# Performance work log

Hardware: AMD Instinct MI355X
Metric: run time of the kernel (lower is better)

The kernel has to match this reference:

```python
import jax, jax.numpy as jnp
import numpy as np

LEAK = 0.1   # LeakyReLU negative slope used by Conv2dBatchLeaky
EPS = 1e-5   # BatchNorm eps (torch default)


def conv_bn_leaky(x, w, gamma, beta, mean, var, stride, pad):
    # Conv2d(bias=False) -> BatchNorm (inference) -> LeakyReLU(0.1)
    y = jax.lax.conv_general_dilated(
        x, w, (stride, stride), [(pad, pad), (pad, pad)],
        dimension_numbers=("NCHW", "OIHW", "NCHW"))
    scale = gamma / jnp.sqrt(var + EPS)
    shift = beta - mean * scale
    y = y * scale[None, :, None, None] + shift[None, :, None, None]
    return jnp.where(y > 0, y, LEAK * y)


def reorg(x, s):
    # lightnet Reorg: exact permutation of the darknet reorg layer
    B, C, H, W = x.shape
    x = x.reshape(B, C, H // s, s, W // s, s)
    x = x.transpose(0, 3, 5, 1, 2, 4)           # (B, s, s, C, H/s, W/s)
    return x.reshape(B, s * s * C, H // s, W // s)


def setup_inputs() -> dict:
    key = jax.random.key(0)
    ks = jax.random.split(key, 13)
    B = 64
    inp = {
        "feat0": jax.random.normal(ks[0], (B, 1024, 19, 19), jnp.float32),
        "feat1": jax.random.normal(ks[1], (B, 512, 38, 38), jnp.float32),
        "w1": jax.random.normal(ks[2], (64, 512, 1, 1), jnp.float32) * 0.05,
        "g1": jax.random.uniform(ks[3], (64,), jnp.float32, 0.5, 1.5),
        "b1": jax.random.normal(ks[4], (64,), jnp.float32) * 0.1,
        "m1": jax.random.normal(ks[5], (64,), jnp.float32) * 0.1,
        "v1": jax.random.uniform(ks[6], (64,), jnp.float32, 0.5, 1.5),
        "w2": jax.random.normal(ks[7], (1024, 1280, 3, 3), jnp.float32) * 0.02,
        "g2": jax.random.uniform(ks[8], (1024,), jnp.float32, 0.5, 1.5),
        "b2": jax.random.normal(ks[9], (1024,), jnp.float32) * 0.1,
        "m2": jax.random.normal(ks[10], (1024,), jnp.float32) * 0.1,
        "v2": jax.random.uniform(ks[11], (1024,), jnp.float32, 0.5, 1.5),
        # meta_state: (num_classes=20, num_anchors*6=30, 1024+1)
        "reweight": jax.random.normal(ks[12], (20, 30, 1025), jnp.float32) * 0.05,
    }
    return inp


def reference(feat0, feat1, w1, g1, b1, m1, v1, w2, g2, b2, m2, v2, reweight):
    # layers[0]: 1x1 ConvBatchLeaky(512->64) + Reorg(2)
    x = conv_bn_leaky(feat1, w1, g1, b1, m1, v1, stride=1, pad=0)
    x = reorg(x, 2)                                  # (B, 256, 19, 19)
    # layers[1]: 3x3 ConvBatchLeaky(1280->1024), pad=1
    cat = jnp.concatenate([x, feat0], axis=1)        # (B, 1280, 19, 19)
    pre = conv_bn_leaky(cat, w2, g2, b2, m2, v2, stride=1, pad=1)  # (B,1024,19,19)
    # get_reweighted_output: per-class dynamic 1x1 conv, batched as one einsum
    cw = reweight[:, :, :-1]                         # (K=20, O=30, 1024)
    cb = reweight[:, :, -1]                          # (K, O)
    det = jnp.einsum("bchw,koc->bkohw", pre, cw) + cb[None, :, :, None, None]
    B, _, _, H, W = det.shape
    return det.reshape(B * 20, 30, H, W)
```

## Files before the change

### kernel.cpp

```cpp
#include <hip/hip_runtime.h>

typedef unsigned short u16;
typedef __attribute__((ext_vector_type(8))) __bf16 bf16x8;
typedef __attribute__((ext_vector_type(4))) float f32x4;

__device__ __forceinline__ u16 f2bf(float f) {
  union { float f; unsigned u; } v; v.f = f;
  unsigned r = v.u + 0x7fffu + ((v.u >> 16) & 1u);
  return (u16)(r >> 16);
}

__device__ __forceinline__ void gld16(const void* g, const void* l) {
  __builtin_amdgcn_global_load_lds((const __attribute__((address_space(1))) void*)g,
                                   (__attribute__((address_space(3))) void*)l, 16, 0, 0);
}


__global__ __launch_bounds__(256) void k_prep_params(
    const float* g1, const float* b1, const float* m1, const float* v1,
    const float* g2, const float* b2, const float* m2, const float* v2,
    const float* rw, float* scale1, float* shift1, float* scale2, float* shift2,
    float* cbf)
{
  int i = blockIdx.x * 256 + threadIdx.x;
  if (i < 64) {
    float s = g1[i] * rsqrtf(v1[i] + 1e-5f);
    scale1[i] = s; shift1[i] = b1[i] - m1[i] * s;
  } else if (i < 1088) {
    int c = i - 64;
    float s = g2[c] * rsqrtf(v2[c] + 1e-5f);
    scale2[c] = s; shift2[c] = b2[c] - m2[c] * s;
  } else if (i < 1728) {
    int n = i - 1088;
    cbf[n] = (n < 600) ? rw[n * 1025 + 1024] : 0.f;
  }
}

__global__ __launch_bounds__(256) void k_cast_w1(const float* w1, u16* w1b) {
  int i = blockIdx.x * 256 + threadIdx.x;
  w1b[i] = f2bf(w1[i]);
}

__global__ __launch_bounds__(256) void k_cast_cwt(const float* rw, u16* cwt) {
  int i = blockIdx.x * 256 + threadIdx.x;
  int n = i >> 10, c = i & 1023;
  cwt[i] = (n < 600) ? f2bf(rw[n * 1025 + c]) : (u16)0;
}

__global__ __launch_bounds__(256) void k_prep_w2(const float* w2, u16* w2t) {
  __shared__ float buf[11520];
  int o = blockIdx.x;
  const float* src = w2 + (size_t)o * 11520;
  for (int i = threadIdx.x; i < 11520; i += 256) buf[i] = src[i];
  __syncthreads();
  for (int t = 0; t < 9; ++t) {
    u16* dst = w2t + ((size_t)t * 1024 + o) * 1280;
    for (int ci = threadIdx.x; ci < 1280; ci += 256) dst[ci] = f2bf(buf[ci * 9 + t]);
  }
}

__global__ __launch_bounds__(256) void k_feat0(const float* feat0, u16* cat) {
  __shared__ float tile[32][33];
  int b = blockIdx.z, c0 = blockIdx.y * 32, p0 = blockIdx.x * 32;
  int tid = threadIdx.x;
  int lo = tid & 31, hi = tid >> 5;
#pragma unroll
  for (int pass = 0; pass < 4; ++pass) {
    int cl = pass * 8 + hi;
    int p = p0 + lo;
    tile[cl][lo] = (p < 361) ? feat0[((size_t)(b * 1024 + c0 + cl)) * 361 + p] : 0.f;
  }
  __syncthreads();
#pragma unroll
  for (int pass = 0; pass < 4; ++pass) {
    int pl = pass * 8 + hi;
    int p = p0 + pl;
    if (p < 361) {
      int h = p / 19, w = p - h * 19;
      cat[(((size_t)b * 21 + 1 + h) * 21 + 1 + w) * 1280 + 256 + c0 + lo] = f2bf(tile[lo][pl]);
    }
  }
}

__global__ __launch_bounds__(256) void k_conv1(const float* feat1, const u16* w1b,
    const float* scale1, const float* shift1, u16* cat)
{
  __shared__ u16 As[128 * 40];
  __shared__ u16 Bs[64 * 32];
  int tid = threadIdx.x;
  int wave = tid >> 6, lane = tid & 63;
  int wr = wave >> 1, wc = wave & 1;
  int lm = lane & 15, lq = lane >> 4;
  int m0 = blockIdx.x * 128;

  int mLoc = tid & 127, cHalf = tid >> 7;
  int mA = m0 + mLoc;
  int bA = mA / 1444, qA = mA - bA * 1444;
  const float* aG = feat1 + ((size_t)bA * 512) * 1444 + qA;

  const u16* bG = w1b + (tid >> 2) * 512 + (tid & 3) * 8;
  char* BsW = (char*)Bs + wave * 1024;

  f32x4 acc[4][2];
#pragma unroll
  for (int i = 0; i < 4; ++i)
#pragma unroll
    for (int j = 0; j < 2; ++j)
#pragma unroll
      for (int r = 0; r < 4; ++r) acc[i][j][r] = 0.f;

  for (int k0 = 0; k0 < 512; k0 += 32) {
    gld16(bG + k0, BsW);
#pragma unroll
    for (int pass = 0; pass < 16; ++pass) {
      int c = pass * 2 + cHalf;
      As[mLoc * 40 + c] = f2bf(aG[(size_t)(k0 + c) * 1444]);
    }
    __syncthreads();
    bf16x8 aF[4], bF[2];
#pragma unroll
    for (int i = 0; i < 4; ++i)
      aF[i] = *(const bf16x8*)(As + (wr * 64 + i * 16 + lm) * 40 + lq * 8);
#pragma unroll
    for (int j = 0; j < 2; ++j)
      bF[j] = *(const bf16x8*)(Bs + (wc * 32 + j * 16 + lm) * 32 + lq * 8);
#pragma unroll
    for (int i = 0; i < 4; ++i)
#pragma unroll
      for (int j = 0; j < 2; ++j)
        acc[i][j] = __builtin_amdgcn_mfma_f32_16x16x32_bf16(aF[i], bF[j], acc[i][j], 0, 0, 0);
    __syncthreads();
  }

  int o0 = wc * 32;
  float sc[2], sh[2];
#pragma unroll
  for (int j = 0; j < 2; ++j) {
    int o = o0 + j * 16 + lm;
    sc[j] = scale1[o]; sh[j] = shift1[o];
  }
#pragma unroll
  for (int i = 0; i < 4; ++i) {
#pragma unroll
    for (int r = 0; r < 4; ++r) {
      int m = m0 + wr * 64 + i * 16 + lq * 4 + r;
      int b = m / 1444, q = m - b * 1444;
      int yy = q / 38, xx = q - yy * 38;
      size_t base = (((size_t)b * 21 + 1 + (yy >> 1)) * 21 + 1 + (xx >> 1)) * 1280
                  + ((yy & 1) * 2 + (xx & 1)) * 64;
#pragma unroll
      for (int j = 0; j < 2; ++j) {
        float v = acc[i][j][r] * sc[j] + sh[j];
        v = v > 0.f ? v : 0.1f * v;
        cat[base + o0 + j * 16 + lm] = f2bf(v);
      }
    }
  }
}

__global__ __launch_bounds__(256) void k_conv2(const u16* cat, const u16* w2t,
    const float* scale2, const float* shift2, u16* pre)
{
  __shared__ u16 As[4096];
  __shared__ u16 Bs[4096];
  int tid = threadIdx.x;
  int wave = tid >> 6, lane = tid & 63;
  int wr = wave >> 1, wc = wave & 1;
  int lm = lane & 15, lq = lane >> 4;
  int n0 = blockIdx.x * 128, m0 = blockIdx.y * 128;

  int r0 = tid >> 2, seg = tid & 3;
  int mA0 = m0 + r0;       if (mA0 > 23103) mA0 = 23103;
  int mA1 = m0 + r0 + 64;  if (mA1 > 23103) mA1 = 23103;
  int b0 = mA0 / 361, p0 = mA0 - b0 * 361, y0 = p0 / 19, x0 = p0 - y0 * 19;
  int b1 = mA1 / 361, p1 = mA1 - b1 * 361, y1 = p1 / 19, x1 = p1 - y1 * 19;
  const u16* aP0 = cat + ((size_t)(b0 * 21 + y0) * 21 + x0) * 1280 + seg * 8;
  const u16* aP1 = cat + ((size_t)(b1 * 21 + y1) * 21 + x1) * 1280 + seg * 8;
  const u16* bP0 = w2t + (size_t)(n0 + r0) * 1280 + seg * 8;
  const u16* bP1 = bP0 + (size_t)64 * 1280;

  char* AsW0 = (char*)As + wave * 1024; char* AsW1 = AsW0 + 4096;
  char* BsW0 = (char*)Bs + wave * 1024; char* BsW1 = BsW0 + 4096;

  f32x4 acc[4][4];
#pragma unroll
  for (int i = 0; i < 4; ++i)
#pragma unroll
    for (int j = 0; j < 4; ++j)
#pragma unroll
      for (int r = 0; r < 4; ++r) acc[i][j][r] = 0.f;

#pragma unroll
  for (int t = 0; t < 9; ++t) {
    const int tapOff = ((t / 3) * 21 + (t % 3)) * 1280;
    const u16* a0 = aP0 + tapOff;
    const u16* a1 = aP1 + tapOff;
    const u16* bb0 = bP0 + (size_t)t * 1310720;
    const u16* bb1 = bP1 + (size_t)t * 1310720;
    for (int k = 0; k < 40; ++k) {
      int co = k * 32;
      gld16(a0 + co, AsW0);
      gld16(a1 + co, AsW1);
      gld16(bb0 + co, BsW0);
      gld16(bb1 + co, BsW1);
      __syncthreads();
      bf16x8 aF[4], bF[4];
#pragma unroll
      for (int i = 0; i < 4; ++i)
        aF[i] = *(const bf16x8*)(As + (wr * 64 + i * 16 + lm) * 32 + lq * 8);
#pragma unroll
      for (int j = 0; j < 4; ++j)
        bF[j] = *(const bf16x8*)(Bs + (wc * 64 + j * 16 + lm) * 32 + lq * 8);
#pragma unroll
      for (int i = 0; i < 4; ++i)
#pragma unroll
        for (int j = 0; j < 4; ++j)
          acc[i][j] = __builtin_amdgcn_mfma_f32_16x16x32_bf16(aF[i], bF[j], acc[i][j], 0, 0, 0);
      __syncthreads();
    }
  }

  int nn[4]; float sc[4], sh[4];
#pragma unroll
  for (int j = 0; j < 4; ++j) {
    nn[j] = n0 + wc * 64 + j * 16 + lm;
    sc[j] = scale2[nn[j]]; sh[j] = shift2[nn[j]];
  }
#pragma unroll
  for (int i = 0; i < 4; ++i) {
#pragma unroll
    for (int r = 0; r < 4; ++r) {
      int m = m0 + wr * 64 + i * 16 + lq * 4 + r;
      if (m < 23104) {
        u16* row = pre + (size_t)m * 1024;
#pragma unroll
        for (int j = 0; j < 4; ++j) {
          float v = acc[i][j][r] * sc[j] + sh[j];
          v = v > 0.f ? v : 0.1f * v;
          row[nn[j]] = f2bf(v);
        }
      }
    }
  }
}

__global__ __launch_bounds__(256) void k_einsum(const u16* pre, const u16* cwt,
    const float* cbf, float* out)
{
  __shared__ u16 As[4096];
  __shared__ u16 Bs[4096];
  int tid = threadIdx.x;
  int wave = tid >> 6, lane = tid & 63;
  int wr = wave >> 1, wc = wave & 1;
  int lm = lane & 15, lq = lane >> 4;
  int n0 = blockIdx.x * 128, m0 = blockIdx.y * 128;

  int r0 = tid >> 2, seg = tid & 3;
  int mA0 = m0 + r0;       if (mA0 > 23103) mA0 = 23103;
  int mA1 = m0 + r0 + 64;  if (mA1 > 23103) mA1 = 23103;
  const u16* aP0 = pre + (size_t)mA0 * 1024 + seg * 8;
  const u16* aP1 = pre + (size_t)mA1 * 1024 + seg * 8;
  const u16* bP0 = cwt + (size_t)(n0 + r0) * 1024 + seg * 8;
  const u16* bP1 = bP0 + (size_t)64 * 1024;

  char* AsW0 = (char*)As + wave * 1024; char* AsW1 = AsW0 + 4096;
  char* BsW0 = (char*)Bs + wave * 1024; char* BsW1 = BsW0 + 4096;

  f32x4 acc[4][4];
#pragma unroll
  for (int i = 0; i < 4; ++i)
#pragma unroll
    for (int j = 0; j < 4; ++j)
#pragma unroll
      for (int r = 0; r < 4; ++r) acc[i][j][r] = 0.f;

  for (int k0 = 0; k0 < 1024; k0 += 32) {
    gld16(aP0 + k0, AsW0);
    gld16(aP1 + k0, AsW1);
    gld16(bP0 + k0, BsW0);
    gld16(bP1 + k0, BsW1);
    __syncthreads();
    bf16x8 aF[4], bF[4];
#pragma unroll
    for (int i = 0; i < 4; ++i)
      aF[i] = *(const bf16x8*)(As + (wr * 64 + i * 16 + lm) * 32 + lq * 8);
#pragma unroll
    for (int j = 0; j < 4; ++j)
      bF[j] = *(const bf16x8*)(Bs + (wc * 64 + j * 16 + lm) * 32 + lq * 8);
#pragma unroll
    for (int i = 0; i < 4; ++i)
#pragma unroll
      for (int j = 0; j < 4; ++j)
        acc[i][j] = __builtin_amdgcn_mfma_f32_16x16x32_bf16(aF[i], bF[j], acc[i][j], 0, 0, 0);
    __syncthreads();
  }

  int nn[4]; float bias[4];
#pragma unroll
  for (int j = 0; j < 4; ++j) {
    nn[j] = n0 + wc * 64 + j * 16 + lm;
    bias[j] = cbf[nn[j]];
  }
#pragma unroll
  for (int i = 0; i < 4; ++i) {
#pragma unroll
    for (int r = 0; r < 4; ++r) {
      int m = m0 + wr * 64 + i * 16 + lq * 4 + r;
      if (m < 23104) {
        int b = m / 361, p = m - b * 361;
        float* orow = out + (size_t)b * 600 * 361 + p;
#pragma unroll
        for (int j = 0; j < 4; ++j) {
          if (nn[j] < 600) orow[(size_t)nn[j] * 361] = acc[i][j][r] + bias[j];
        }
      }
    }
  }
}


extern "C" void kernel_launch(void* const* d_in, const int* in_sizes, int n_in,
                              void* d_out, int out_size, void* d_ws, size_t ws_size,
                              hipStream_t stream) {
  const float* feat0 = (const float*)d_in[0];
  const float* feat1 = (const float*)d_in[1];
  const float* w1 = (const float*)d_in[2];
  const float* g1 = (const float*)d_in[3];
  const float* b1 = (const float*)d_in[4];
  const float* m1 = (const float*)d_in[5];
  const float* v1 = (const float*)d_in[6];
  const float* w2 = (const float*)d_in[7];
  const float* g2 = (const float*)d_in[8];
  const float* b2 = (const float*)d_in[9];
  const float* m2 = (const float*)d_in[10];
  const float* v2 = (const float*)d_in[11];
  const float* rw = (const float*)d_in[12];
  float* out = (float*)d_out;

  char* ws = (char*)d_ws;
  u16* cat    = (u16*)(ws);
  u16* w2t    = (u16*)(ws + 72253440);
  u16* pre    = (u16*)(ws + 95846400);
  u16* w1b    = (u16*)(ws + 143163392);
  u16* cwt    = (u16*)(ws + 143228928);
  float* scale1 = (float*)(ws + 144539648);
  float* shift1 = (float*)(ws + 144539904);
  float* scale2 = (float*)(ws + 144540160);
  float* shift2 = (float*)(ws + 144544256);
  float* cbf    = (float*)(ws + 144548352);

  hipMemsetAsync(cat, 0, 72253440, stream);

  k_prep_params<<<7, 256, 0, stream>>>(g1, b1, m1, v1, g2, b2, m2, v2, rw,
                                       scale1, shift1, scale2, shift2, cbf);
  k_cast_w1<<<128, 256, 0, stream>>>(w1, w1b);
  k_cast_cwt<<<2560, 256, 0, stream>>>(rw, cwt);
  k_prep_w2<<<1024, 256, 0, stream>>>(w2, w2t);
  k_feat0<<<dim3(12, 32, 64), 256, 0, stream>>>(feat0, cat);
  k_conv1<<<722, 256, 0, stream>>>(feat1, w1b, scale1, shift1, cat);
  k_conv2<<<dim3(8, 181), 256, 0, stream>>>(cat, w2t, scale2, shift2, pre);
  k_einsum<<<dim3(5, 181), 256, 0, stream>>>(pre, cwt, cbf, out);
}
```

Measured before the change: 1.348 ms.

## Merge dx taps into contiguous K, double K-step in conv2, transpose einsum operands

The conv2 weights are reordered so the three dx taps of each kernel row sit next to each other (K=3840 per dy). This works because neighbouring x pixels in the padded NHWC cat buffer are contiguous, so each dy becomes a single long GEMM K loop. The conv2 main loop now loads 64 K-elements per barrier pair instead of 32, which halves the synchronisation count and doubles LDS usage. The einsum swaps operands so class weights are the M dimension and pixels the N dimension. Output writes then become coalesced along pixels instead of strided by 361, and the grid changes to match.

Measured after the change: 1.219 ms. -9.6%, faster.

```diff
diff --git a/kernel.cpp b/kernel.cpp
--- a/kernel.cpp
+++ b/kernel.cpp
@@ -54,7 +54,8 @@
   for (int i = threadIdx.x; i < 11520; i += 256) buf[i] = src[i];
   __syncthreads();
   for (int t = 0; t < 9; ++t) {
-    u16* dst = w2t + ((size_t)t * 1024 + o) * 1280;
+    int dy = t / 3, dx = t - dy * 3;
+    u16* dst = w2t + ((size_t)dy * 1024 + o) * 3840 + dx * 1280;
     for (int ci = threadIdx.x; ci < 1280; ci += 256) dst[ci] = f2bf(buf[ci * 9 + t]);
   }
 }
@@ -161,26 +162,31 @@
 __global__ __launch_bounds__(256) void k_conv2(const u16* cat, const u16* w2t,
     const float* scale2, const float* shift2, u16* pre)
 {
-  __shared__ u16 As[4096];
-  __shared__ u16 Bs[4096];
+  __shared__ u16 As[8192];
+  __shared__ u16 Bs[8192];
   int tid = threadIdx.x;
   int wave = tid >> 6, lane = tid & 63;
   int wr = wave >> 1, wc = wave & 1;
   int lm = lane & 15, lq = lane >> 4;
   int n0 = blockIdx.x * 128, m0 = blockIdx.y * 128;
 
-  int r0 = tid >> 2, seg = tid & 3;
-  int mA0 = m0 + r0;       if (mA0 > 23103) mA0 = 23103;
-  int mA1 = m0 + r0 + 64;  if (mA1 > 23103) mA1 = 23103;
-  int b0 = mA0 / 361, p0 = mA0 - b0 * 361, y0 = p0 / 19, x0 = p0 - y0 * 19;
-  int b1 = mA1 / 361, p1 = mA1 - b1 * 361, y1 = p1 / 19, x1 = p1 - y1 * 19;
-  const u16* aP0 = cat + ((size_t)(b0 * 21 + y0) * 21 + x0) * 1280 + seg * 8;
-  const u16* aP1 = cat + ((size_t)(b1 * 21 + y1) * 21 + x1) * 1280 + seg * 8;
-  const u16* bP0 = w2t + (size_t)(n0 + r0) * 1280 + seg * 8;
-  const u16* bP1 = bP0 + (size_t)64 * 1280;
-
-  char* AsW0 = (char*)As + wave * 1024; char* AsW1 = AsW0 + 4096;
-  char* BsW0 = (char*)Bs + wave * 1024; char* BsW1 = BsW0 + 4096;
+  int rIn = lane >> 2;
+  int kseg = (lane & 3) * 8;
+  int rowLo = wave * 16 + rIn;
+
+  int mLo = m0 + rowLo;       if (mLo > 23103) mLo = 23103;
+  int mHi = m0 + rowLo + 64;  if (mHi > 23103) mHi = 23103;
+  int bL = mLo / 361, pL = mLo - bL * 361, yL = pL / 19, xL = pL - yL * 19;
+  int bH = mHi / 361, pH = mHi - bH * 361, yH = pH / 19, xH = pH - yH * 19;
+  const u16* aLo = cat + ((size_t)(bL * 21 + yL) * 21 + xL) * 1280 + kseg;
+  const u16* aHi = cat + ((size_t)(bH * 21 + yH) * 21 + xH) * 1280 + kseg;
+  const u16* bLo = w2t + (size_t)(n0 + rowLo) * 3840 + kseg;
+  const u16* bHi = bLo + (size_t)64 * 3840;
+
+  u16* asJ0 = As + wave * 512;          u16* asJ1 = As + (4 + wave) * 512;
+  u16* asJ2 = As + 4096 + wave * 512;   u16* asJ3 = As + 4096 + (4 + wave) * 512;
+  u16* bsJ0 = Bs + wave * 512;          u16* bsJ1 = Bs + (4 + wave) * 512;
+  u16* bsJ2 = Bs + 4096 + wave * 512;   u16* bsJ3 = Bs + 4096 + (4 + wave) * 512;
 
   f32x4 acc[4][4];
 #pragma unroll
@@ -190,32 +196,36 @@
 #pragma unroll
       for (int r = 0; r < 4; ++r) acc[i][j][r] = 0.f;
 
-#pragma unroll
-  for (int t = 0; t < 9; ++t) {
-    const int tapOff = ((t / 3) * 21 + (t % 3)) * 1280;
-    const u16* a0 = aP0 + tapOff;
-    const u16* a1 = aP1 + tapOff;
-    const u16* bb0 = bP0 + (size_t)t * 1310720;
-    const u16* bb1 = bP1 + (size_t)t * 1310720;
-    for (int k = 0; k < 40; ++k) {
-      int co = k * 32;
-      gld16(a0 + co, AsW0);
-      gld16(a1 + co, AsW1);
-      gld16(bb0 + co, BsW0);
-      gld16(bb1 + co, BsW1);
+  for (int dy = 0; dy < 3; ++dy) {
+    const u16* a0 = aLo + dy * 26880;
+    const u16* a1 = aHi + dy * 26880;
+    const u16* b0 = bLo + (size_t)dy * 3932160;
+    const u16* b1 = bHi + (size_t)dy * 3932160;
+    for (int k0 = 0; k0 < 3840; k0 += 64) {
+      gld16(a0 + k0,      asJ0);
+      gld16(a1 + k0,      asJ1);
+      gld16(a0 + k0 + 32, asJ2);
+      gld16(a1 + k0 + 32, asJ3);
+      gld16(b0 + k0,      bsJ0);
+      gld16(b1 + k0,      bsJ1);
+      gld16(b0 + k0 + 32, bsJ2);
+      gld16(b1 + k0 + 32, bsJ3);
       __syncthreads();
-      bf16x8 aF[4], bF[4];
-#pragma unroll
-      for (int i = 0; i < 4; ++i)
-        aF[i] = *(const bf16x8*)(As + (wr * 64 + i * 16 + lm) * 32 + lq * 8);
-#pragma unroll
-      for (int j = 0; j < 4; ++j)
-        bF[j] = *(const bf16x8*)(Bs + (wc * 64 + j * 16 + lm) * 32 + lq * 8);
-#pragma unroll
-      for (int i = 0; i < 4; ++i)
+#pragma unroll
+      for (int kk = 0; kk < 2; ++kk) {
+        bf16x8 aF[4], bF[4];
+#pragma unroll
+        for (int i = 0; i < 4; ++i)
+          aF[i] = *(const bf16x8*)(As + kk * 4096 + (wr * 64 + i * 16 + lm) * 32 + lq * 8);
 #pragma unroll
         for (int j = 0; j < 4; ++j)
-          acc[i][j] = __builtin_amdgcn_mfma_f32_16x16x32_bf16(aF[i], bF[j], acc[i][j], 0, 0, 0);
+          bF[j] = *(const bf16x8*)(Bs + kk * 4096 + (wc * 64 + j * 16 + lm) * 32 + lq * 8);
+#pragma unroll
+        for (int i = 0; i < 4; ++i)
+#pragma unroll
+          for (int j = 0; j < 4; ++j)
+            acc[i][j] = __builtin_amdgcn_mfma_f32_16x16x32_bf16(aF[i], bF[j], acc[i][j], 0, 0, 0);
+      }
       __syncthreads();
     }
   }
@@ -253,18 +263,19 @@
   int wave = tid >> 6, lane = tid & 63;
   int wr = wave >> 1, wc = wave & 1;
   int lm = lane & 15, lq = lane >> 4;
-  int n0 = blockIdx.x * 128, m0 = blockIdx.y * 128;
-
-  int r0 = tid >> 2, seg = tid & 3;
-  int mA0 = m0 + r0;       if (mA0 > 23103) mA0 = 23103;
-  int mA1 = m0 + r0 + 64;  if (mA1 > 23103) mA1 = 23103;
-  const u16* aP0 = pre + (size_t)mA0 * 1024 + seg * 8;
-  const u16* aP1 = pre + (size_t)mA1 * 1024 + seg * 8;
-  const u16* bP0 = cwt + (size_t)(n0 + r0) * 1024 + seg * 8;
-  const u16* bP1 = bP0 + (size_t)64 * 1024;
-
-  char* AsW0 = (char*)As + wave * 1024; char* AsW1 = AsW0 + 4096;
-  char* BsW0 = (char*)Bs + wave * 1024; char* BsW1 = BsW0 + 4096;
+  int n0 = blockIdx.x * 128;
+  int m0 = blockIdx.y * 128;
+
+  int r0 = tid >> 2, seg = (tid & 3) * 8;
+  const u16* aP0 = cwt + (size_t)(m0 + r0) * 1024 + seg;
+  const u16* aP1 = aP0 + (size_t)64 * 1024;
+  int q0 = n0 + r0;       if (q0 > 23103) q0 = 23103;
+  int q1 = n0 + r0 + 64;  if (q1 > 23103) q1 = 23103;
+  const u16* bP0 = pre + (size_t)q0 * 1024 + seg;
+  const u16* bP1 = pre + (size_t)q1 * 1024 + seg;
+
+  char* AsW = (char*)As + wave * 1024;
+  char* BsW = (char*)Bs + wave * 1024;
 
   f32x4 acc[4][4];
 #pragma unroll
@@ -275,10 +286,10 @@
       for (int r = 0; r < 4; ++r) acc[i][j][r] = 0.f;
 
   for (int k0 = 0; k0 < 1024; k0 += 32) {
-    gld16(aP0 + k0, AsW0);
-    gld16(aP1 + k0, AsW1);
-    gld16(bP0 + k0, BsW0);
-    gld16(bP1 + k0, BsW1);
+    gld16(aP0 + k0, AsW);
+    gld16(aP1 + k0, AsW + 4096);
+    gld16(bP0 + k0, BsW);
+    gld16(bP1 + k0, BsW + 4096);
     __syncthreads();
     bf16x8 aF[4], bF[4];
 #pragma unroll
@@ -295,23 +306,24 @@
     __syncthreads();
   }
 
-  int nn[4]; float bias[4];
+  int pix[4], pb[4], pp[4];
 #pragma unroll
   for (int j = 0; j < 4; ++j) {
-    nn[j] = n0 + wc * 64 + j * 16 + lm;
-    bias[j] = cbf[nn[j]];
+    pix[j] = n0 + wc * 64 + j * 16 + lm;
+    int b = pix[j] / 361;
+    pb[j] = b; pp[j] = pix[j] - b * 361;
   }
 #pragma unroll
   for (int i = 0; i < 4; ++i) {
 #pragma unroll
     for (int r = 0; r < 4; ++r) {
-      int m = m0 + wr * 64 + i * 16 + lq * 4 + r;
-      if (m < 23104) {
-        int b = m / 361, p = m - b * 361;
-        float* orow = out + (size_t)b * 600 * 361 + p;
+      int cw = m0 + wr * 64 + i * 16 + lq * 4 + r;
+      if (cw < 600) {
+        float bias = cbf[cw];
 #pragma unroll
         for (int j = 0; j < 4; ++j) {
-          if (nn[j] < 600) orow[(size_t)nn[j] * 361] = acc[i][j][r] + bias[j];
+          if (pix[j] < 23104)
+            out[(size_t)pb[j] * 216600 + (size_t)cw * 361 + pp[j]] = acc[i][j][r] + bias;
         }
       }
     }
@@ -359,5 +371,5 @@
   k_feat0<<<dim3(12, 32, 64), 256, 0, stream>>>(feat0, cat);
   k_conv1<<<722, 256, 0, stream>>>(feat1, w1b, scale1, shift1, cat);
   k_conv2<<<dim3(8, 181), 256, 0, stream>>>(cat, w2t, scale2, shift2, pre);
-  k_einsum<<<dim3(5, 181), 256, 0, stream>>>(pre, cwt, cbf, out);
-}
+  k_einsum<<<dim3(181, 5), 256, 0, stream>>>(pre, cwt, cbf, out);
+}
```
